# Kernel tuning notes

Hardware: AMD Instinct MI355X
Metric: run time of the kernel (lower is better)

The kernel has to match this reference:

```python
import jax, jax.numpy as jnp
import numpy as np

N_BASIS = 32
MAX_SCALE = 4.0
N_ANCHOR = 2048   # i / Vi axis
N_POINTS = 8192   # j / Vj axis


def setup_inputs() -> dict:
    key = jax.random.key(0)
    k1, k2, k3 = jax.random.split(key, 3)
    f = jax.random.normal(k1, (N_POINTS, 1), dtype=jnp.float32)
    coords = jax.random.normal(k2, (N_POINTS, 3), dtype=jnp.float32)
    anchor_coords = jax.random.normal(k3, (N_ANCHOR, 3), dtype=jnp.float32)
    # buffers from __init__: scales = linspace(0, max_scale, n_basis+1)[1:]
    scales = jnp.linspace(0.0, MAX_SCALE, N_BASIS + 1)[1:]
    mu = 1.0 / scales                       # [n_basis] decay rates B
    norms = 8.0 * jnp.pi * scales ** 3      # [n_basis] normalizers
    return {"f": f, "coords": coords, "anchor_coords": anchor_coords,
            "mu": mu, "norms": norms}


def reference(f, coords, anchor_coords, mu, norms):
    # KeOps formula: Sum_j Exp(-B * Norm2(X-Y)) * F   (Norm2 = Euclidean norm)
    diff = anchor_coords[:, None, :] - coords[None, :, :]   # [N, M, 3]
    d = jnp.sqrt(jnp.sum(diff * diff, axis=-1))             # [N, M] pairwise distances
    fj = f[:, 0]                                            # [M]

    # scan over the (small) basis axis so we never materialize [n_basis, N, M]
    def body(_, mu_b):
        return None, jnp.exp(-mu_b * d) @ fj                # [N]

    _, out = jax.lax.scan(body, None, mu)                   # [n_basis, N]
    return out.T / norms                                    # [N, n_basis]
```

## Files before the change

### kernel.cpp

```cpp
#include <hip/hip_runtime.h>
#include <math.h>

#define NB      32
#define NPOINTS 8192
#define NANCHOR 2048
#define TPB     256
#define NMOM    17
#define NITER   (NPOINTS / (4 * TPB))

typedef float v2f __attribute__((ext_vector_type(2)));

struct Coefs { float c[NB][NMOM]; };

__device__ __forceinline__ float fexp2_neg(float x) {
    float r; asm("v_exp_f32 %0, -%1" : "=v"(r) : "v"(x)); return r;
}
__device__ __forceinline__ float fsqrt(float x) {
    float r; asm("v_sqrt_f32 %0, %1" : "=v"(r) : "v"(x)); return r;
}

__global__ __launch_bounds__(TPB) void expo_pool_kernel(
    const float* __restrict__ f,
    const float* __restrict__ coords,
    const float* __restrict__ anchors,
    const Coefs C,
    float* __restrict__ out) {

    const int a = blockIdx.x;
    const int t = threadIdx.x;
    const float ax = anchors[3 * a + 0];
    const float ay = anchors[3 * a + 1];
    const float az = anchors[3 * a + 2];

    constexpr float SC = (float)(1.0 / (16.0 * 0.6931471805599453 * 0.6931471805599453));

    float m[NMOM];
#pragma unroll
    for (int c = 0; c < NMOM; ++c) m[c] = 0.0f;

#pragma unroll 1
    for (int i = 0; i < NITER; ++i) {
        const int p0 = (2 * i) * TPB + t;
        const int p1 = (2 * i + 1) * TPB + t;
        const v2f* cp0 = (const v2f*)(coords + 6 * p0);
        const v2f* cp1 = (const v2f*)(coords + 6 * p1);
        const v2f A0 = cp0[0], B0 = cp0[1], G0 = cp0[2];
        const v2f A1 = cp1[0], B1 = cp1[1], G1 = cp1[2];
        const v2f fv0 = *(const v2f*)(f + 2 * p0);
        const v2f fv1 = *(const v2f*)(f + 2 * p1);

        const float cx[4] = {A0.x, B0.y, A1.x, B1.y};
        const float cy[4] = {A0.y, G0.x, A1.y, G1.x};
        const float cz[4] = {B0.x, G0.y, B1.x, G1.y};
        const float fk[4] = {fv0.x, fv0.y, fv1.x, fv1.y};

        float u[4], v[4], Tp[4], Tc[4];
#pragma unroll
        for (int k = 0; k < 4; ++k) {
            const float dx = ax - cx[k];
            const float dy = ay - cy[k];
            const float dz = az - cz[k];
            const float q  = fmaf(dx, dx, fmaf(dy, dy, dz * dz));
            const float dp = fsqrt(SC * q);
            const float x  = fexp2_neg(dp);
            u[k]  = fmaf(2.0f, x, -1.0f);
            v[k]  = u[k] + u[k];
            Tp[k] = 1.0f;
            Tc[k] = u[k];
        }

        m[0] += (fk[0] + fk[1]) + (fk[2] + fk[3]);
#pragma unroll
        for (int k = 0; k < 4; ++k) m[1] = fmaf(u[k], fk[k], m[1]);

#pragma unroll
        for (int c = 2; c < NMOM; ++c) {
#pragma unroll
            for (int k = 0; k < 4; ++k) {
                const float Tn = fmaf(v[k], Tc[k], -Tp[k]);
                m[c] = fmaf(Tn, fk[k], m[c]);
                Tp[k] = Tc[k];
                Tc[k] = Tn;
            }
        }
    }

#pragma unroll
    for (int c = 0; c < NMOM; ++c) {
        float val = m[c];
#pragma unroll
        for (int off = 32; off > 0; off >>= 1)
            val += __shfl_xor(val, off, 64);
        m[c] = val;
    }

    __shared__ float red[TPB / 64][NMOM];
    const int wave = t >> 6;
    const int lane = t & 63;
    if (lane == 0) {
#pragma unroll
        for (int c = 0; c < NMOM; ++c) red[wave][c] = m[c];
    }
    __syncthreads();

    if (t < NB) {
        float o = 0.0f;
#pragma unroll
        for (int c = 0; c < NMOM; ++c) {
            const float mc = (red[0][c] + red[1][c]) + (red[2][c] + red[3][c]);
            o = fmaf(C.c[t][c], mc, o);
        }
        out[a * NB + t] = o;
    }
}

extern "C" void kernel_launch(void* const* d_in, const int* in_sizes, int n_in,
                              void* d_out, int out_size, void* d_ws, size_t ws_size,
                              hipStream_t stream) {
    const float* f       = (const float*)d_in[0];
    const float* coords  = (const float*)d_in[1];
    const float* anchors = (const float*)d_in[2];
    float* out           = (float*)d_out;

    Coefs C;
    const int N = NMOM;
    for (int b = 0; b < NB; ++b) {
        const float scale = (float)(b + 1) * 0.125f;
        const float muf   = 1.0f / scale;
        const double alpha = 4.0 * (double)muf;
        const float s3    = (scale * scale) * scale;
        const float normf = (float)(8.0 * M_PI) * s3;

        double g[NMOM];
        for (int mm = 0; mm < N; ++mm) {
            const double th = M_PI * ((double)mm + 0.5) / (double)N;
            const double x  = 0.5 * (cos(th) + 1.0);
            g[mm] = pow(x, alpha);
        }
        for (int c = 0; c < N; ++c) {
            double s = 0.0;
            for (int mm = 0; mm < N; ++mm)
                s += g[mm] * cos((double)c * M_PI * ((double)mm + 0.5) / (double)N);
            s *= 2.0 / (double)N;
            if (c == 0) s *= 0.5;
            C.c[b][c] = (float)(s / (double)normf);
        }
    }

    expo_pool_kernel<<<NANCHOR, TPB, 0, stream>>>(f, coords, anchors, C, out);
}
```

Before: 81.17 us.

## Split moment accumulation into smaller blocks and move basis combine to second kernel

The moment kernel now uses two 128-thread blocks per anchor, each covering half the points, and writes per-wave partial moments to workspace without a block barrier. A separate kernel sums the four partials and applies the Chebyshev coefficients for every anchor/basis pair. This aims to improve scheduling granularity and remove the shared-memory barrier in the tail, at the cost of an extra launch and a global-memory round trip.

```diff
diff --git a/kernel.cpp b/kernel.cpp
--- a/kernel.cpp
+++ b/kernel.cpp
@@ -4,9 +4,11 @@
 #define NB      32
 #define NPOINTS 8192
 #define NANCHOR 2048
-#define TPB     256
 #define NMOM    17
-#define NITER   (NPOINTS / (4 * TPB))
+
+#define P1_TPB  128
+#define P1_NBLK (NANCHOR * 2)
+#define P1_ITER 8
 
 typedef float v2f __attribute__((ext_vector_type(2)));
 
@@ -19,15 +21,17 @@
     float r; asm("v_sqrt_f32 %0, %1" : "=v"(r) : "v"(x)); return r;
 }
 
-__global__ __launch_bounds__(TPB) void expo_pool_kernel(
+__global__ __launch_bounds__(P1_TPB) void moments_kernel(
     const float* __restrict__ f,
     const float* __restrict__ coords,
     const float* __restrict__ anchors,
-    const Coefs C,
-    float* __restrict__ out) {
+    float* __restrict__ ws) {
 
-    const int a = blockIdx.x;
-    const int t = threadIdx.x;
+    const int bid  = blockIdx.x;
+    const int a    = bid >> 1;
+    const int half = bid & 1;
+    const int t    = threadIdx.x;
+
     const float ax = anchors[3 * a + 0];
     const float ay = anchors[3 * a + 1];
     const float az = anchors[3 * a + 2];
@@ -39,15 +43,15 @@
     for (int c = 0; c < NMOM; ++c) m[c] = 0.0f;
 
 #pragma unroll 1
-    for (int i = 0; i < NITER; ++i) {
-        const int p0 = (2 * i) * TPB + t;
-        const int p1 = (2 * i + 1) * TPB + t;
-        const v2f* cp0 = (const v2f*)(coords + 6 * p0);
-        const v2f* cp1 = (const v2f*)(coords + 6 * p1);
+    for (int i = 0; i < P1_ITER; ++i) {
+        const int pr0 = half * 2048 + i * 256 + t;
+        const int pr1 = pr0 + 128;
+        const v2f* cp0 = (const v2f*)(coords + 6 * pr0);
+        const v2f* cp1 = (const v2f*)(coords + 6 * pr1);
         const v2f A0 = cp0[0], B0 = cp0[1], G0 = cp0[2];
         const v2f A1 = cp1[0], B1 = cp1[1], G1 = cp1[2];
-        const v2f fv0 = *(const v2f*)(f + 2 * p0);
-        const v2f fv1 = *(const v2f*)(f + 2 * p1);
+        const v2f fv0 = *(const v2f*)(f + 2 * pr0);
+        const v2f fv1 = *(const v2f*)(f + 2 * pr1);
 
         const float cx[4] = {A0.x, B0.y, A1.x, B1.y};
         const float cy[4] = {A0.y, G0.x, A1.y, G1.x};
@@ -94,24 +98,32 @@
         m[c] = val;
     }
 
-    __shared__ float red[TPB / 64][NMOM];
     const int wave = t >> 6;
     const int lane = t & 63;
     if (lane == 0) {
+        float* dst = ws + (size_t)((a << 2) + (half << 1) + wave) * NMOM;
 #pragma unroll
-        for (int c = 0; c < NMOM; ++c) red[wave][c] = m[c];
+        for (int c = 0; c < NMOM; ++c) dst[c] = m[c];
     }
-    __syncthreads();
+}
 
-    if (t < NB) {
-        float o = 0.0f;
+__global__ __launch_bounds__(256) void combine_kernel(
+    const float* __restrict__ ws,
+    const Coefs C,
+    float* __restrict__ out) {
+
+    const int gid = blockIdx.x * 256 + threadIdx.x;
+    const int a = gid >> 5;
+    const int b = gid & 31;
+
+    const float* w = ws + (size_t)(a << 2) * NMOM;
+    float o = 0.0f;
 #pragma unroll
-        for (int c = 0; c < NMOM; ++c) {
-            const float mc = (red[0][c] + red[1][c]) + (red[2][c] + red[3][c]);
-            o = fmaf(C.c[t][c], mc, o);
-        }
-        out[a * NB + t] = o;
+    for (int c = 0; c < NMOM; ++c) {
+        const float mc = (w[c] + w[NMOM + c]) + (w[2 * NMOM + c] + w[3 * NMOM + c]);
+        o = fmaf(C.c[b][c], mc, o);
     }
+    out[gid] = o;
 }
 
 extern "C" void kernel_launch(void* const* d_in, const int* in_sizes, int n_in,
@@ -121,6 +133,7 @@
     const float* coords  = (const float*)d_in[1];
     const float* anchors = (const float*)d_in[2];
     float* out           = (float*)d_out;
+    float* ws            = (float*)d_ws;
 
     Coefs C;
     const int N = NMOM;
@@ -147,5 +160,6 @@
         }
     }
 
-    expo_pool_kernel<<<NANCHOR, TPB, 0, stream>>>(f, coords, anchors, C, out);
+    moments_kernel<<<P1_NBLK, P1_TPB, 0, stream>>>(f, coords, anchors, ws);
+    combine_kernel<<<NANCHOR * NB / 256, 256, 0, stream>>>(ws, C, out);
 }
```

New measurement: 83.12 us. 1.02x slower.

## Process two anchors per block to reuse point loads and shared m0

Applied to the files above, without the earlier changes.

Each block now handles two anchors, so every loaded point's coordinates and f value serve two distance/Chebyshev evaluations. Points are fetched as contiguous 16-byte vectors, four consecutive points per thread. The grid is halved, the f-sum moment is shared between both anchors, and the final reduction writes two output rows. This cuts global load traffic and per-point overhead per anchor, but roughly doubles the accumulator registers and gives fewer blocks for occupancy.

```diff
diff --git a/kernel.cpp b/kernel.cpp
--- a/kernel.cpp
+++ b/kernel.cpp
@@ -8,7 +8,7 @@
 #define NMOM    17
 #define NITER   (NPOINTS / (4 * TPB))
 
-typedef float v2f __attribute__((ext_vector_type(2)));
+typedef float v4f __attribute__((ext_vector_type(4)));
 
 struct Coefs { float c[NB][NMOM]; };
 
@@ -26,91 +26,133 @@
     const Coefs C,
     float* __restrict__ out) {
 
-    const int a = blockIdx.x;
-    const int t = threadIdx.x;
-    const float ax = anchors[3 * a + 0];
-    const float ay = anchors[3 * a + 1];
-    const float az = anchors[3 * a + 2];
+    const int bid = blockIdx.x;
+    const int a0  = 2 * bid;
+    const int t   = threadIdx.x;
+
+    const float ax0 = anchors[3 * a0 + 0], ay0 = anchors[3 * a0 + 1], az0 = anchors[3 * a0 + 2];
+    const float ax1 = anchors[3 * a0 + 3], ay1 = anchors[3 * a0 + 4], az1 = anchors[3 * a0 + 5];
 
     constexpr float SC = (float)(1.0 / (16.0 * 0.6931471805599453 * 0.6931471805599453));
 
-    float m[NMOM];
+    float m0 = 0.0f;
+    float mA[NMOM - 1], mB[NMOM - 1];
 #pragma unroll
-    for (int c = 0; c < NMOM; ++c) m[c] = 0.0f;
+    for (int c = 0; c < NMOM - 1; ++c) { mA[c] = 0.0f; mB[c] = 0.0f; }
 
 #pragma unroll 1
     for (int i = 0; i < NITER; ++i) {
-        const int p0 = (2 * i) * TPB + t;
-        const int p1 = (2 * i + 1) * TPB + t;
-        const v2f* cp0 = (const v2f*)(coords + 6 * p0);
-        const v2f* cp1 = (const v2f*)(coords + 6 * p1);
-        const v2f A0 = cp0[0], B0 = cp0[1], G0 = cp0[2];
-        const v2f A1 = cp1[0], B1 = cp1[1], G1 = cp1[2];
-        const v2f fv0 = *(const v2f*)(f + 2 * p0);
-        const v2f fv1 = *(const v2f*)(f + 2 * p1);
+        const int p4 = i * TPB + t;
+        const v4f* cp = (const v4f*)(coords + 12 * p4);
+        const v4f L0 = cp[0];
+        const v4f L1 = cp[1];
+        const v4f L2 = cp[2];
+        const v4f fv = *(const v4f*)(f + 4 * p4);
 
-        const float cx[4] = {A0.x, B0.y, A1.x, B1.y};
-        const float cy[4] = {A0.y, G0.x, A1.y, G1.x};
-        const float cz[4] = {B0.x, G0.y, B1.x, G1.y};
-        const float fk[4] = {fv0.x, fv0.y, fv1.x, fv1.y};
+        const float cx[4] = {L0.x, L0.w, L1.z, L2.y};
+        const float cy[4] = {L0.y, L1.x, L1.w, L2.z};
+        const float cz[4] = {L0.z, L1.y, L2.x, L2.w};
+        const float fk[4] = {fv.x, fv.y, fv.z, fv.w};
 
-        float u[4], v[4], Tp[4], Tc[4];
-#pragma unroll
-        for (int k = 0; k < 4; ++k) {
-            const float dx = ax - cx[k];
-            const float dy = ay - cy[k];
-            const float dz = az - cz[k];
-            const float q  = fmaf(dx, dx, fmaf(dy, dy, dz * dz));
-            const float dp = fsqrt(SC * q);
-            const float x  = fexp2_neg(dp);
-            u[k]  = fmaf(2.0f, x, -1.0f);
-            v[k]  = u[k] + u[k];
-            Tp[k] = 1.0f;
-            Tc[k] = u[k];
-        }
+        m0 += (fk[0] + fk[1]) + (fk[2] + fk[3]);
 
-        m[0] += (fk[0] + fk[1]) + (fk[2] + fk[3]);
-#pragma unroll
-        for (int k = 0; k < 4; ++k) m[1] = fmaf(u[k], fk[k], m[1]);
-
-#pragma unroll
-        for (int c = 2; c < NMOM; ++c) {
+        {
+            float u[4], v[4], Tp[4], Tc[4];
 #pragma unroll
             for (int k = 0; k < 4; ++k) {
-                const float Tn = fmaf(v[k], Tc[k], -Tp[k]);
-                m[c] = fmaf(Tn, fk[k], m[c]);
-                Tp[k] = Tc[k];
-                Tc[k] = Tn;
+                const float dx = ax0 - cx[k];
+                const float dy = ay0 - cy[k];
+                const float dz = az0 - cz[k];
+                const float q  = fmaf(dx, dx, fmaf(dy, dy, dz * dz));
+                const float x  = fexp2_neg(fsqrt(SC * q));
+                u[k]  = fmaf(2.0f, x, -1.0f);
+                v[k]  = u[k] + u[k];
+                Tp[k] = 1.0f;
+                Tc[k] = u[k];
+                mA[0] = fmaf(u[k], fk[k], mA[0]);
+            }
+#pragma unroll
+            for (int c = 1; c < NMOM - 1; ++c) {
+#pragma unroll
+                for (int k = 0; k < 4; ++k) {
+                    const float Tn = fmaf(v[k], Tc[k], -Tp[k]);
+                    mA[c] = fmaf(Tn, fk[k], mA[c]);
+                    Tp[k] = Tc[k];
+                    Tc[k] = Tn;
+                }
+            }
+        }
+        {
+            float u[4], v[4], Tp[4], Tc[4];
+#pragma unroll
+            for (int k = 0; k < 4; ++k) {
+                const float dx = ax1 - cx[k];
+                const float dy = ay1 - cy[k];
+                const float dz = az1 - cz[k];
+                const float q  = fmaf(dx, dx, fmaf(dy, dy, dz * dz));
+                const float x  = fexp2_neg(fsqrt(SC * q));
+                u[k]  = fmaf(2.0f, x, -1.0f);
+                v[k]  = u[k] + u[k];
+                Tp[k] = 1.0f;
+                Tc[k] = u[k];
+                mB[0] = fmaf(u[k], fk[k], mB[0]);
+            }
+#pragma unroll
+            for (int c = 1; c < NMOM - 1; ++c) {
+#pragma unroll
+                for (int k = 0; k < 4; ++k) {
+                    const float Tn = fmaf(v[k], Tc[k], -Tp[k]);
+                    mB[c] = fmaf(Tn, fk[k], mB[c]);
+                    Tp[k] = Tc[k];
+                    Tc[k] = Tn;
+                }
             }
         }
     }
 
+    {
+        float val = m0;
 #pragma unroll
-    for (int c = 0; c < NMOM; ++c) {
-        float val = m[c];
+        for (int off = 32; off > 0; off >>= 1) val += __shfl_xor(val, off, 64);
+        m0 = val;
+    }
 #pragma unroll
-        for (int off = 32; off > 0; off >>= 1)
-            val += __shfl_xor(val, off, 64);
-        m[c] = val;
+    for (int c = 0; c < NMOM - 1; ++c) {
+        float va = mA[c], vb = mB[c];
+#pragma unroll
+        for (int off = 32; off > 0; off >>= 1) {
+            va += __shfl_xor(va, off, 64);
+            vb += __shfl_xor(vb, off, 64);
+        }
+        mA[c] = va; mB[c] = vb;
     }
 
-    __shared__ float red[TPB / 64][NMOM];
+    __shared__ float red[TPB / 64][1 + 2 * (NMOM - 1)];
     const int wave = t >> 6;
     const int lane = t & 63;
     if (lane == 0) {
+        red[wave][0] = m0;
 #pragma unroll
-        for (int c = 0; c < NMOM; ++c) red[wave][c] = m[c];
+        for (int c = 0; c < NMOM - 1; ++c) {
+            red[wave][1 + c]            = mA[c];
+            red[wave][1 + (NMOM - 1) + c] = mB[c];
+        }
     }
     __syncthreads();
 
-    if (t < NB) {
-        float o = 0.0f;
+    if (t < 64) {
+        const int b   = t & 31;
+        const int sel = t >> 5;
+        const int off = 1 + sel * (NMOM - 1);
+        const float mc0 = (red[0][0] + red[1][0]) + (red[2][0] + red[3][0]);
+        float o = C.c[b][0] * mc0;
 #pragma unroll
-        for (int c = 0; c < NMOM; ++c) {
-            const float mc = (red[0][c] + red[1][c]) + (red[2][c] + red[3][c]);
-            o = fmaf(C.c[t][c], mc, o);
+        for (int c = 1; c < NMOM; ++c) {
+            const float mc = (red[0][off + c - 1] + red[1][off + c - 1]) +
+                             (red[2][off + c - 1] + red[3][off + c - 1]);
+            o = fmaf(C.c[b][c], mc, o);
         }
-        out[a * NB + t] = o;
+        out[(a0 + sel) * NB + b] = o;
     }
 }
 
@@ -147,5 +189,5 @@
         }
     }
 
-    expo_pool_kernel<<<NANCHOR, TPB, 0, stream>>>(f, coords, anchors, C, out);
+    expo_pool_kernel<<<NANCHOR / 2, TPB, 0, stream>>>(f, coords, anchors, C, out);
 }
```

Result: no change. 81.18 us (+0.0%).
